# Performance work log

Hardware: AMD Instinct MI355X
Metric: run time of the kernel (lower is better)

Reference implementation:

```python
import jax, jax.numpy as jnp
import numpy as np

SIZE = (96, 160, 160)  # (D, H, W) from init_kwargs


def grid_sample_3d(inp, grid, padding_mode):
    """PyTorch-semantics 3D grid_sample, trilinear, align_corners=True.
    inp: (B, C, D, H, W); grid: (B, Do, Ho, Wo, 3) with grid[...,0]=x(W), [...,1]=y(H), [...,2]=z(D).
    """
    B, C, D, H, W = inp.shape
    x = (grid[..., 0] + 1.0) * 0.5 * (W - 1)
    y = (grid[..., 1] + 1.0) * 0.5 * (H - 1)
    z = (grid[..., 2] + 1.0) * 0.5 * (D - 1)
    if padding_mode == 'border':
        x = jnp.clip(x, 0.0, W - 1)
        y = jnp.clip(y, 0.0, H - 1)
        z = jnp.clip(z, 0.0, D - 1)
    x0f, y0f, z0f = jnp.floor(x), jnp.floor(y), jnp.floor(z)
    fx, fy, fz = x - x0f, y - y0f, z - z0f
    x0, y0, z0 = x0f.astype(jnp.int32), y0f.astype(jnp.int32), z0f.astype(jnp.int32)
    x1, y1, z1 = x0 + 1, y0 + 1, z0 + 1

    flat = inp.reshape(B, C, D * H * W)
    Do, Ho, Wo = grid.shape[1:4]
    N = Do * Ho * Wo

    def corner(zi, yi, xi, w):
        if padding_mode == 'zeros':
            valid = ((zi >= 0) & (zi < D) & (yi >= 0) & (yi < H) & (xi >= 0) & (xi < W))
            w = w * valid.astype(inp.dtype)
        zi = jnp.clip(zi, 0, D - 1)
        yi = jnp.clip(yi, 0, H - 1)
        xi = jnp.clip(xi, 0, W - 1)
        idx = ((zi * H + yi) * W + xi).reshape(B, 1, N)
        vals = jnp.take_along_axis(flat, idx, axis=2).reshape(B, C, Do, Ho, Wo)
        return vals * w[:, None]

    out = (corner(z0, y0, x0, (1 - fz) * (1 - fy) * (1 - fx))
           + corner(z0, y0, x1, (1 - fz) * (1 - fy) * fx)
           + corner(z0, y1, x0, (1 - fz) * fy * (1 - fx))
           + corner(z0, y1, x1, (1 - fz) * fy * fx)
           + corner(z1, y0, x0, fz * (1 - fy) * (1 - fx))
           + corner(z1, y0, x1, fz * (1 - fy) * fx)
           + corner(z1, y1, x0, fz * fy * (1 - fx))
           + corner(z1, y1, x1, fz * fy * fx))
    return out


def make_grid():
    D, H, W = SIZE
    g = jnp.stack(jnp.meshgrid(jnp.arange(D), jnp.arange(H), jnp.arange(W), indexing='ij'))
    return g[None].astype(jnp.float32)  # (1, 3, D, H, W)


def setup_inputs() -> dict:
    key = jax.random.key(0)
    k1, k2 = jax.random.split(key)
    D, H, W = SIZE
    src = jax.random.normal(k1, (1, 1, D, H, W), dtype=jnp.float32)
    flows = jax.random.normal(k2, (3, 1, 3, D, H, W), dtype=jnp.float32)
    range_flow = jnp.float32(0.4)
    return {"src": src, "flows": flows, "range_flow": range_flow}


def reference(src, flows, range_flow):
    D, H, W = SIZE
    grid = make_grid()  # (1, 3, D, H, W)
    shape = jnp.array([D, H, W], dtype=jnp.float32).reshape(-1, 1, 1, 1)
    acc = jnp.zeros_like(grid)
    for i in range(flows.shape[0]):  # small fixed number of flow stages
        flow = flows[i]
        ng = 2.0 * (grid / shape) - 1.0
        warped = grid_sample_3d(flow, jnp.transpose(ng, (0, 2, 3, 4, 1)), 'border')
        acc = acc + warped
    final = grid + acc * range_flow
    denom = jnp.array([D - 1, H - 1, W - 1], dtype=jnp.float32).reshape(-1, 1, 1, 1)
    final = 2.0 * (final / denom - 0.5)
    fg = jnp.transpose(final, (0, 2, 3, 4, 1))
    return grid_sample_3d(src, fg, 'zeros')
```

## Files before the change

kernel.cpp:

```cpp
#include <hip/hip_runtime.h>
#include <stdint.h>

constexpr int Dz = 96, Hy = 160, Wx = 160;
constexpr int NVOX = Dz * Hy * Wx;

constexpr int ZW = 6, YW = 3, XP = 56;
constexpr int ROWS = ZW * YW;
constexpr int NCHUNK = ROWS * 14;
constexpr int UI = 4;
constexpr int WBUF = UI * 64 * 4;

#define WAIT_LGKM() do { asm volatile("s_waitcnt lgkmcnt(0)" ::: "memory"); \
                         __builtin_amdgcn_sched_barrier(0); } while (0)
#define FENCE() __builtin_amdgcn_sched_barrier(0)

__global__ __launch_bounds__(128) void st_fused_kernel(
    const float* __restrict__ src,
    const float* __restrict__ flows,
    const float* __restrict__ rfp,
    float* __restrict__ out)
{
    __shared__ float raw[2][WBUF];
    const int t = threadIdx.x;
    const int v = t >> 6;
    const int lane = t & 63;

    const int bid = blockIdx.x;
    const int swz = (bid & 7) * 300 + (bid >> 3);
    const int wid = swz * 2 + v;
    const int wt = wid % 20;
    const int rest = wid / 20;
    const int dt = rest % 3;
    const int hp = rest / 3;
    const int w0w = wt * 8, d0 = dt * 32, h0 = hp * 2;
    const float rf = *rfp;

    const int Z0w = (19 * w0w) >> 5;
    const int X0 = 53 * dt;
    const int X0a = X0 & ~3;
    const int YB = (159 * h0) / 160;

    const char* ap[UI];
    {
        const char* fb = (const char*)flows + ((size_t)YB * Wx + X0a) * 4;
#pragma unroll
        for (int u = 0; u < UI; ++u) {
            int c = u * 64 + lane;
            if (c >= NCHUNK) c = NCHUNK - 1;
            int row = c / 14, ch = c - row * 14;
            int zr = row / 3, yr = row - zr * 3;
            ap[u] = fb + ((size_t)((Z0w + zr) * Hy + yr) * Wx) * 4 + ch * 16;
        }
    }

    float4 nxt[3][UI];
    auto issue_ch = [&]() {
#pragma unroll
        for (int i = 0; i < 3; ++i)
#pragma unroll
            for (int u = 0; u < UI; ++u)
                nxt[i][u] = *(const float4*)(ap[u] + (size_t)i * (3u * NVOX * 4u));
#pragma unroll
        for (int u = 0; u < UI; ++u) ap[u] += (size_t)NVOX * 4;
    };
    float* const lb = &raw[v][0];
    auto commit_ch = [&]() {
        float4* lb4 = (float4*)lb;
#pragma unroll
        for (int u = 0; u < UI; ++u) {
            float4 s;
            s.x = (nxt[0][u].x + nxt[1][u].x) + nxt[2][u].x;
            s.y = (nxt[0][u].y + nxt[1][u].y) + nxt[2][u].y;
            s.z = (nxt[0][u].z + nxt[1][u].z) + nxt[2][u].z;
            s.w = (nxt[0][u].w + nxt[1][u].w) + nxt[2][u].w;
            lb4[u * 64 + lane] = s;
        }
    };

    const int dl = lane & 31;
    const int half = lane >> 5;
    const int d = d0 + dl;

    const float xf = (float)(53 * d) * (1.0f / 32.0f);
    const int   x0i = (int)xf;
    const float fx  = xf - (float)x0i;
    const int   xx  = x0i - X0a;
    const float wxa = 1.0f - fx, wxb = fx;

    int rowoff[4];
    float wkz[4][4];
    {
        int zzk[4]; float wz0k[4], wz1k[4];
#pragma unroll
        for (int k = 0; k < 4; ++k) {
            const int w = w0w + 4 * half + k;
            const float zf = (float)(19 * w) * (1.0f / 32.0f);
            const int z0i = (int)zf;
            const float fz = zf - (float)z0i;
            zzk[k] = z0i - Z0w;
            wz0k[k] = 1.0f - fz; wz1k[k] = fz;
        }
        const int zz0 = zzk[0];
#pragma unroll
        for (int r = 0; r < 4; ++r) {
            rowoff[r] = min(zz0 + r, ZW - 1) * (YW * XP);
#pragma unroll
            for (int k = 0; k < 4; ++k) {
                const int rel = zzk[k] - zz0;
                wkz[r][k] = (rel == r) ? wz0k[k] : ((rel == r - 1) ? wz1k[k] : 0.0f);
            }
        }
    }

    float wyr[2][3];
#pragma unroll
    for (int j = 0; j < 2; ++j) {
        const int h = h0 + j;
        const float yf = (float)h * (159.0f / 160.0f);
        const int y0i = (int)yf;
        const float fy = yf - (float)y0i;
        const int yrel = y0i - YB;
        const float a = 1.0f - fy, b = fy;
        wyr[j][0] = (yrel == 0) ? a : 0.0f;
        wyr[j][1] = (yrel == 0) ? b : a;
        wyr[j][2] = (yrel == 0) ? 0.0f : b;
    }

    auto compute = [&](float (&acc)[4][2]) {
#pragma unroll
        for (int yy = 0; yy < 3; ++yy) {
            float zv0 = 0.f, zv1 = 0.f, zv2 = 0.f, zv3 = 0.f;
#pragma unroll
            for (int r = 0; r < 4; ++r) {
                const float* p = lb + rowoff[r] + yy * XP + xx;
                const float xv = wxa * p[0] + wxb * p[1];
                zv0 += wkz[r][0] * xv;
                zv1 += wkz[r][1] * xv;
                zv2 += wkz[r][2] * xv;
                zv3 += wkz[r][3] * xv;
            }
            acc[0][0] += wyr[0][yy] * zv0; acc[0][1] += wyr[1][yy] * zv0;
            acc[1][0] += wyr[0][yy] * zv1; acc[1][1] += wyr[1][yy] * zv1;
            acc[2][0] += wyr[0][yy] * zv2; acc[2][1] += wyr[1][yy] * zv2;
            acc[3][0] += wyr[0][yy] * zv3; acc[3][1] += wyr[1][yy] * zv3;
        }
    };

    float accA[4][2], accB[4][2], accC[4][2];
#pragma unroll
    for (int k = 0; k < 4; ++k)
#pragma unroll
        for (int j = 0; j < 2; ++j) { accA[k][j] = 0.f; accB[k][j] = 0.f; accC[k][j] = 0.f; }

    issue_ch();
    commit_ch();
    issue_ch();
    compute(accA);
    FENCE();
    commit_ch();
    issue_ch();
    compute(accB);
    FENCE();
    commit_ch();
    compute(accC);

    float* tr = &raw[v][0];
#pragma unroll
    for (int j = 0; j < 2; ++j) {
        const int h = h0 + j;
#pragma unroll
        for (int k = 0; k < 4; ++k) {
            const int w = w0w + 4 * half + k;
            const float f0 = (float)d + accA[k][j] * rf;
            const float f1 = (float)h + accB[k][j] * rf;
            const float f2 = (float)w + accC[k][j] * rf;

            const float xs = f0 * (159.0f / 95.0f);
            const float ys = f1;
            const float zs = f2 * (95.0f / 159.0f);

            const float xf0 = floorf(xs), yf0 = floorf(ys), zf0 = floorf(zs);
            const float gx = xs - xf0, gy = ys - yf0, gz = zs - zf0;
            const int xi0 = (int)xf0, yi0 = (int)yf0, zi0 = (int)zf0;

            const int xc = min(max(xi0, 0), Wx - 2);
            const bool sx0 = (xi0 == xc);
            const float wx0m = ((unsigned)xi0 < (unsigned)Wx) ? (1.0f - gx) : 0.0f;
            const float wx1m = ((unsigned)(xi0 + 1) < (unsigned)Wx) ? gx : 0.0f;

            const int yc0 = min(max(yi0, 0), Hy - 1);
            const int yc1 = min(max(yi0 + 1, 0), Hy - 1);
            const int zc0 = min(max(zi0, 0), Dz - 1);
            const int zc1 = min(max(zi0 + 1, 0), Dz - 1);
            const float wy0m = ((unsigned)yi0 < (unsigned)Hy) ? (1.0f - gy) : 0.0f;
            const float wy1m = ((unsigned)(yi0 + 1) < (unsigned)Hy) ? gy : 0.0f;
            const float wz0m = ((unsigned)zi0 < (unsigned)Dz) ? (1.0f - gz) : 0.0f;
            const float wz1m = ((unsigned)(zi0 + 1) < (unsigned)Dz) ? gz : 0.0f;

            const float w00 = wz0m * wy0m, w01 = wz0m * wy1m;
            const float w10 = wz1m * wy0m, w11 = wz1m * wy1m;

            float r = 0.0f;
            auto rowadd = [&](int zc, int yc, float wt) {
                const float* p = src + ((size_t)zc * Hy + yc) * Wx + xc;
                const float va = p[0], vb = p[1];
                const float s0 = sx0 ? va : vb;
                const float s1 = sx0 ? vb : va;
                r += wt * (wx0m * s0 + wx1m * s1);
            };
            rowadd(zc0, yc0, w00);
            rowadd(zc0, yc1, w01);
            rowadd(zc1, yc0, w10);
            rowadd(zc1, yc1, w11);

            tr[j * 288 + dl * 9 + 4 * half + k] = r;
        }
    }
    WAIT_LGKM();

    const int rrow = lane >> 3;
    const int rcol = lane & 7;
#pragma unroll
    for (int j = 0; j < 2; ++j)
#pragma unroll
        for (int m = 0; m < 4; ++m) {
            const int dr = m * 8 + rrow;
            out[((size_t)(d0 + dr) * Hy + (h0 + j)) * Wx + (w0w + rcol)] =
                tr[j * 288 + dr * 9 + rcol];
        }
}

extern "C" void kernel_launch(void* const* d_in, const int* in_sizes, int n_in,
                              void* d_out, int out_size, void* d_ws, size_t ws_size,
                              hipStream_t stream) {
    const float* src   = (const float*)d_in[0];
    const float* flows = (const float*)d_in[1];
    const float* rfp   = (const float*)d_in[2];
    float* out = (float*)d_out;

    st_fused_kernel<<<dim3(2400), 128, 0, stream>>>(src, flows, rfp, out);
}
```

Before: 30.20 us.

## Halve per-wave output rows to one h-row, doubling grid and shrinking flow window

Each wave now produces one output h-row instead of two. The flow staging window drops from 3 y-rows to 2, which cuts per-lane loads (UI 4→3), accumulator registers and interpolation work per wave. The grid doubles to 4800 blocks, and the staging loads are reorganised into a two-buffer software pipeline built from macros, with the wave id made scalar via readfirstlane. In exchange, the overlapping y-row of flows is fetched redundantly by neighbouring waves, raising total global traffic, and there are more blocks to schedule.

```diff
diff --git a/kernel.cpp b/kernel.cpp
--- a/kernel.cpp
+++ b/kernel.cpp
@@ -4,10 +4,10 @@
 constexpr int Dz = 96, Hy = 160, Wx = 160;
 constexpr int NVOX = Dz * Hy * Wx;
 
-constexpr int ZW = 6, YW = 3, XP = 56;
+constexpr int ZW = 6, YW = 2, XP = 56;
 constexpr int ROWS = ZW * YW;
 constexpr int NCHUNK = ROWS * 14;
-constexpr int UI = 4;
+constexpr int UI = 3;
 constexpr int WBUF = UI * 64 * 4;
 
 #define WAIT_LGKM() do { asm volatile("s_waitcnt lgkmcnt(0)" ::: "memory"); \
@@ -22,17 +22,17 @@
 {
     __shared__ float raw[2][WBUF];
     const int t = threadIdx.x;
-    const int v = t >> 6;
     const int lane = t & 63;
 
     const int bid = blockIdx.x;
-    const int swz = (bid & 7) * 300 + (bid >> 3);
-    const int wid = swz * 2 + v;
+    const int swz = (bid & 7) * 600 + (bid >> 3);
+    const int wid = __builtin_amdgcn_readfirstlane(swz * 2 + (t >> 6));
     const int wt = wid % 20;
     const int rest = wid / 20;
     const int dt = rest % 3;
-    const int hp = rest / 3;
-    const int w0w = wt * 8, d0 = dt * 32, h0 = hp * 2;
+    const int h0 = rest / 3;
+    const int w0w = wt * 8, d0 = dt * 32;
+    const int v = t >> 6;
     const float rf = *rfp;
 
     const int Z0w = (19 * w0w) >> 5;
@@ -48,34 +48,25 @@
             int c = u * 64 + lane;
             if (c >= NCHUNK) c = NCHUNK - 1;
             int row = c / 14, ch = c - row * 14;
-            int zr = row / 3, yr = row - zr * 3;
-            ap[u] = fb + ((size_t)((Z0w + zr) * Hy + yr) * Wx) * 4 + ch * 16;
-        }
-    }
-
-    float4 nxt[3][UI];
-    auto issue_ch = [&]() {
-#pragma unroll
-        for (int i = 0; i < 3; ++i)
-#pragma unroll
-            for (int u = 0; u < UI; ++u)
-                nxt[i][u] = *(const float4*)(ap[u] + (size_t)i * (3u * NVOX * 4u));
-#pragma unroll
-        for (int u = 0; u < UI; ++u) ap[u] += (size_t)NVOX * 4;
-    };
+            int zr = row >> 1, yr = row & 1;
+            ap[u] = fb + ((size_t)(zr * Hy + yr) * Wx + (size_t)Z0w * Hy * Wx) * 4 + ch * 16;
+        }
+    }
+
     float* const lb = &raw[v][0];
-    auto commit_ch = [&]() {
-        float4* lb4 = (float4*)lb;
-#pragma unroll
-        for (int u = 0; u < UI; ++u) {
-            float4 s;
-            s.x = (nxt[0][u].x + nxt[1][u].x) + nxt[2][u].x;
-            s.y = (nxt[0][u].y + nxt[1][u].y) + nxt[2][u].y;
-            s.z = (nxt[0][u].z + nxt[1][u].z) + nxt[2][u].z;
-            s.w = (nxt[0][u].w + nxt[1][u].w) + nxt[2][u].w;
-            lb4[u * 64 + lane] = s;
-        }
-    };
+    float4 bA[3], bB[3];
+#define LOADB(SET, U) do { \
+    _Pragma("unroll") \
+    for (int i = 0; i < 3; ++i) \
+        SET[i] = *(const float4*)(ap[U] + (size_t)i * (3u * NVOX * 4u)); \
+    ap[U] += (size_t)NVOX * 4; } while (0)
+#define STOREB(SET, U) do { \
+    float4 s; \
+    s.x = (SET[0].x + SET[1].x) + SET[2].x; \
+    s.y = (SET[0].y + SET[1].y) + SET[2].y; \
+    s.z = (SET[0].z + SET[1].z) + SET[2].z; \
+    s.w = (SET[0].w + SET[1].w) + SET[2].w; \
+    ((float4*)lb)[(U) * 64 + lane] = s; } while (0)
 
     const int dl = lane & 31;
     const int half = lane >> 5;
@@ -112,23 +103,12 @@
         }
     }
 
-    float wyr[2][3];
-#pragma unroll
-    for (int j = 0; j < 2; ++j) {
-        const int h = h0 + j;
-        const float yf = (float)h * (159.0f / 160.0f);
-        const int y0i = (int)yf;
-        const float fy = yf - (float)y0i;
-        const int yrel = y0i - YB;
-        const float a = 1.0f - fy, b = fy;
-        wyr[j][0] = (yrel == 0) ? a : 0.0f;
-        wyr[j][1] = (yrel == 0) ? b : a;
-        wyr[j][2] = (yrel == 0) ? 0.0f : b;
-    }
-
-    auto compute = [&](float (&acc)[4][2]) {
-#pragma unroll
-        for (int yy = 0; yy < 3; ++yy) {
+    const float fy = (float)h0 * (159.0f / 160.0f) - (float)YB;
+    const float wy0 = 1.0f - fy, wy1 = fy;
+
+    auto compute = [&](float (&acc)[4]) {
+#pragma unroll
+        for (int yy = 0; yy < 2; ++yy) {
             float zv0 = 0.f, zv1 = 0.f, zv2 = 0.f, zv3 = 0.f;
 #pragma unroll
             for (int r = 0; r < 4; ++r) {
@@ -139,95 +119,93 @@
                 zv2 += wkz[r][2] * xv;
                 zv3 += wkz[r][3] * xv;
             }
-            acc[0][0] += wyr[0][yy] * zv0; acc[0][1] += wyr[1][yy] * zv0;
-            acc[1][0] += wyr[0][yy] * zv1; acc[1][1] += wyr[1][yy] * zv1;
-            acc[2][0] += wyr[0][yy] * zv2; acc[2][1] += wyr[1][yy] * zv2;
-            acc[3][0] += wyr[0][yy] * zv3; acc[3][1] += wyr[1][yy] * zv3;
+            const float wy = yy ? wy1 : wy0;
+            acc[0] += wy * zv0;
+            acc[1] += wy * zv1;
+            acc[2] += wy * zv2;
+            acc[3] += wy * zv3;
         }
     };
 
-    float accA[4][2], accB[4][2], accC[4][2];
-#pragma unroll
-    for (int k = 0; k < 4; ++k)
-#pragma unroll
-        for (int j = 0; j < 2; ++j) { accA[k][j] = 0.f; accB[k][j] = 0.f; accC[k][j] = 0.f; }
-
-    issue_ch();
-    commit_ch();
-    issue_ch();
+    float accA[4] = {0.f, 0.f, 0.f, 0.f};
+    float accB[4] = {0.f, 0.f, 0.f, 0.f};
+    float accC[4] = {0.f, 0.f, 0.f, 0.f};
+
+    LOADB(bA, 0); LOADB(bB, 1);
+    STOREB(bA, 0); LOADB(bA, 2);
+    STOREB(bB, 1); STOREB(bA, 2);
+    LOADB(bA, 0); LOADB(bB, 1);
     compute(accA);
     FENCE();
-    commit_ch();
-    issue_ch();
+    STOREB(bA, 0); LOADB(bA, 2);
+    STOREB(bB, 1); STOREB(bA, 2);
+    LOADB(bA, 0); LOADB(bB, 1);
     compute(accB);
     FENCE();
-    commit_ch();
+    STOREB(bA, 0); LOADB(bA, 2);
+    STOREB(bB, 1); STOREB(bA, 2);
     compute(accC);
+#undef LOADB
+#undef STOREB
 
     float* tr = &raw[v][0];
 #pragma unroll
-    for (int j = 0; j < 2; ++j) {
-        const int h = h0 + j;
-#pragma unroll
-        for (int k = 0; k < 4; ++k) {
-            const int w = w0w + 4 * half + k;
-            const float f0 = (float)d + accA[k][j] * rf;
-            const float f1 = (float)h + accB[k][j] * rf;
-            const float f2 = (float)w + accC[k][j] * rf;
-
-            const float xs = f0 * (159.0f / 95.0f);
-            const float ys = f1;
-            const float zs = f2 * (95.0f / 159.0f);
-
-            const float xf0 = floorf(xs), yf0 = floorf(ys), zf0 = floorf(zs);
-            const float gx = xs - xf0, gy = ys - yf0, gz = zs - zf0;
-            const int xi0 = (int)xf0, yi0 = (int)yf0, zi0 = (int)zf0;
-
-            const int xc = min(max(xi0, 0), Wx - 2);
-            const bool sx0 = (xi0 == xc);
-            const float wx0m = ((unsigned)xi0 < (unsigned)Wx) ? (1.0f - gx) : 0.0f;
-            const float wx1m = ((unsigned)(xi0 + 1) < (unsigned)Wx) ? gx : 0.0f;
-
-            const int yc0 = min(max(yi0, 0), Hy - 1);
-            const int yc1 = min(max(yi0 + 1, 0), Hy - 1);
-            const int zc0 = min(max(zi0, 0), Dz - 1);
-            const int zc1 = min(max(zi0 + 1, 0), Dz - 1);
-            const float wy0m = ((unsigned)yi0 < (unsigned)Hy) ? (1.0f - gy) : 0.0f;
-            const float wy1m = ((unsigned)(yi0 + 1) < (unsigned)Hy) ? gy : 0.0f;
-            const float wz0m = ((unsigned)zi0 < (unsigned)Dz) ? (1.0f - gz) : 0.0f;
-            const float wz1m = ((unsigned)(zi0 + 1) < (unsigned)Dz) ? gz : 0.0f;
-
-            const float w00 = wz0m * wy0m, w01 = wz0m * wy1m;
-            const float w10 = wz1m * wy0m, w11 = wz1m * wy1m;
-
-            float r = 0.0f;
-            auto rowadd = [&](int zc, int yc, float wt) {
-                const float* p = src + ((size_t)zc * Hy + yc) * Wx + xc;
-                const float va = p[0], vb = p[1];
-                const float s0 = sx0 ? va : vb;
-                const float s1 = sx0 ? vb : va;
-                r += wt * (wx0m * s0 + wx1m * s1);
-            };
-            rowadd(zc0, yc0, w00);
-            rowadd(zc0, yc1, w01);
-            rowadd(zc1, yc0, w10);
-            rowadd(zc1, yc1, w11);
-
-            tr[j * 288 + dl * 9 + 4 * half + k] = r;
-        }
+    for (int k = 0; k < 4; ++k) {
+        const int w = w0w + 4 * half + k;
+        const float f0 = (float)d + accA[k] * rf;
+        const float f1 = (float)h0 + accB[k] * rf;
+        const float f2 = (float)w + accC[k] * rf;
+
+        const float xs = f0 * (159.0f / 95.0f);
+        const float ys = f1;
+        const float zs = f2 * (95.0f / 159.0f);
+
+        const float xf0 = floorf(xs), yf0 = floorf(ys), zf0 = floorf(zs);
+        const float gx = xs - xf0, gy = ys - yf0, gz = zs - zf0;
+        const int xi0 = (int)xf0, yi0 = (int)yf0, zi0 = (int)zf0;
+
+        const int xc = min(max(xi0, 0), Wx - 2);
+        const bool sx0 = (xi0 == xc);
+        const float wx0m = ((unsigned)xi0 < (unsigned)Wx) ? (1.0f - gx) : 0.0f;
+        const float wx1m = ((unsigned)(xi0 + 1) < (unsigned)Wx) ? gx : 0.0f;
+
+        const int yc0 = min(max(yi0, 0), Hy - 1);
+        const int yc1 = min(max(yi0 + 1, 0), Hy - 1);
+        const int zc0 = min(max(zi0, 0), Dz - 1);
+        const int zc1 = min(max(zi0 + 1, 0), Dz - 1);
+        const float wy0m = ((unsigned)yi0 < (unsigned)Hy) ? (1.0f - gy) : 0.0f;
+        const float wy1m = ((unsigned)(yi0 + 1) < (unsigned)Hy) ? gy : 0.0f;
+        const float wz0m = ((unsigned)zi0 < (unsigned)Dz) ? (1.0f - gz) : 0.0f;
+        const float wz1m = ((unsigned)(zi0 + 1) < (unsigned)Dz) ? gz : 0.0f;
+
+        const float w00 = wz0m * wy0m, w01 = wz0m * wy1m;
+        const float w10 = wz1m * wy0m, w11 = wz1m * wy1m;
+
+        float r = 0.0f;
+        auto rowadd = [&](int zc, int yc, float wt) {
+            const float* p = src + ((size_t)zc * Hy + yc) * Wx + xc;
+            const float va = p[0], vb = p[1];
+            const float s0 = sx0 ? va : vb;
+            const float s1 = sx0 ? vb : va;
+            r += wt * (wx0m * s0 + wx1m * s1);
+        };
+        rowadd(zc0, yc0, w00);
+        rowadd(zc0, yc1, w01);
+        rowadd(zc1, yc0, w10);
+        rowadd(zc1, yc1, w11);
+
+        tr[dl * 9 + 4 * half + k] = r;
     }
     WAIT_LGKM();
 
     const int rrow = lane >> 3;
     const int rcol = lane & 7;
 #pragma unroll
-    for (int j = 0; j < 2; ++j)
-#pragma unroll
-        for (int m = 0; m < 4; ++m) {
-            const int dr = m * 8 + rrow;
-            out[((size_t)(d0 + dr) * Hy + (h0 + j)) * Wx + (w0w + rcol)] =
-                tr[j * 288 + dr * 9 + rcol];
-        }
+    for (int m = 0; m < 4; ++m) {
+        const int dr = m * 8 + rrow;
+        out[((size_t)(d0 + dr) * Hy + h0) * Wx + (w0w + rcol)] =
+            tr[dr * 9 + rcol];
+    }
 }
 
 extern "C" void kernel_launch(void* const* d_in, const int* in_sizes, int n_in,
@@ -238,5 +216,5 @@
     const float* rfp   = (const float*)d_in[2];
     float* out = (float*)d_out;
 
-    st_fused_kernel<<<dim3(2400), 128, 0, stream>>>(src, flows, rfp, out);
+    st_fused_kernel<<<dim3(4800), 128, 0, stream>>>(src, flows, rfp, out);
 }
```

Result: no change. 30.63 us (+1.4%).

## Stage all three flow channels into separate LDS buffers instead of software pipelining

Applied to the files above, without the earlier changes.

Replaces the hand-scheduled issue/commit/compute pipeline, which reused one LDS buffer per wave, with three per-channel LDS buffers. All flow loads and sums are written up front, and the three compute passes follow. This lets the compiler schedule the global loads freely and removes the sched_barrier fences, at the cost of tripling LDS usage (about 24 KB per block), which may lower occupancy. It also marks the wave index as uniform with readfirstlane so the index math can run on the scalar unit.

```diff
diff --git a/kernel.cpp b/kernel.cpp
--- a/kernel.cpp
+++ b/kernel.cpp
@@ -12,7 +12,6 @@
 
 #define WAIT_LGKM() do { asm volatile("s_waitcnt lgkmcnt(0)" ::: "memory"); \
                          __builtin_amdgcn_sched_barrier(0); } while (0)
-#define FENCE() __builtin_amdgcn_sched_barrier(0)
 
 __global__ __launch_bounds__(128) void st_fused_kernel(
     const float* __restrict__ src,
@@ -20,14 +19,14 @@
     const float* __restrict__ rfp,
     float* __restrict__ out)
 {
-    __shared__ float raw[2][WBUF];
+    __shared__ float raw[2][3][WBUF];
     const int t = threadIdx.x;
     const int v = t >> 6;
     const int lane = t & 63;
 
     const int bid = blockIdx.x;
     const int swz = (bid & 7) * 300 + (bid >> 3);
-    const int wid = swz * 2 + v;
+    const int wid = __builtin_amdgcn_readfirstlane(swz * 2 + v);
     const int wt = wid % 20;
     const int rest = wid / 20;
     const int dt = rest % 3;
@@ -53,29 +52,22 @@
         }
     }
 
-    float4 nxt[3][UI];
-    auto issue_ch = [&]() {
-#pragma unroll
-        for (int i = 0; i < 3; ++i)
-#pragma unroll
-            for (int u = 0; u < UI; ++u)
-                nxt[i][u] = *(const float4*)(ap[u] + (size_t)i * (3u * NVOX * 4u));
-#pragma unroll
-        for (int u = 0; u < UI; ++u) ap[u] += (size_t)NVOX * 4;
-    };
-    float* const lb = &raw[v][0];
-    auto commit_ch = [&]() {
-        float4* lb4 = (float4*)lb;
+#pragma unroll
+    for (int c = 0; c < 3; ++c) {
+        float4* lb4 = (float4*)&raw[v][c][0];
 #pragma unroll
         for (int u = 0; u < UI; ++u) {
+            const float4 s0 = *(const float4*)(ap[u] + (size_t)(0 + c) * NVOX * 4);
+            const float4 s1 = *(const float4*)(ap[u] + (size_t)(3 + c) * NVOX * 4);
+            const float4 s2 = *(const float4*)(ap[u] + (size_t)(6 + c) * NVOX * 4);
             float4 s;
-            s.x = (nxt[0][u].x + nxt[1][u].x) + nxt[2][u].x;
-            s.y = (nxt[0][u].y + nxt[1][u].y) + nxt[2][u].y;
-            s.z = (nxt[0][u].z + nxt[1][u].z) + nxt[2][u].z;
-            s.w = (nxt[0][u].w + nxt[1][u].w) + nxt[2][u].w;
+            s.x = (s0.x + s1.x) + s2.x;
+            s.y = (s0.y + s1.y) + s2.y;
+            s.z = (s0.z + s1.z) + s2.z;
+            s.w = (s0.w + s1.w) + s2.w;
             lb4[u * 64 + lane] = s;
         }
-    };
+    }
 
     const int dl = lane & 31;
     const int half = lane >> 5;
@@ -126,7 +118,7 @@
         wyr[j][2] = (yrel == 0) ? 0.0f : b;
     }
 
-    auto compute = [&](float (&acc)[4][2]) {
+    auto compute = [&](const float* lb, float (&acc)[4][2]) {
 #pragma unroll
         for (int yy = 0; yy < 3; ++yy) {
             float zv0 = 0.f, zv1 = 0.f, zv2 = 0.f, zv3 = 0.f;
@@ -152,19 +144,11 @@
 #pragma unroll
         for (int j = 0; j < 2; ++j) { accA[k][j] = 0.f; accB[k][j] = 0.f; accC[k][j] = 0.f; }
 
-    issue_ch();
-    commit_ch();
-    issue_ch();
-    compute(accA);
-    FENCE();
-    commit_ch();
-    issue_ch();
-    compute(accB);
-    FENCE();
-    commit_ch();
-    compute(accC);
-
-    float* tr = &raw[v][0];
+    compute(&raw[v][0][0], accA);
+    compute(&raw[v][1][0], accB);
+    compute(&raw[v][2][0], accC);
+
+    float* tr = &raw[v][0][0];
 #pragma unroll
     for (int j = 0; j < 2; ++j) {
         const int h = h0 + j;
```

After: 30.69 us. Within noise of the previous version (+1.6%).
